# Optimization experiments

Measured on AMD Instinct MI355X. Metric: run time of the kernel, lower is better.

Reference implementation:

```python
import jax, jax.numpy as jnp
import numpy as np

HEADS = 8
HEAD_DIM = 64
SCALE = HEAD_DIM ** -0.5


def setup_inputs() -> dict:
    key = jax.random.key(0)
    ks = jax.random.split(key, 5)
    d_model, inner = 1024, HEADS * HEAD_DIM  # 512
    x = jax.random.normal(ks[0], (2, 2048, d_model), dtype=jnp.float32)
    # torch Linear weights stored pre-transposed as [in, out]
    Wq = jax.random.normal(ks[1], (d_model, inner), dtype=jnp.float32) * (d_model ** -0.5)
    Wkv = jax.random.normal(ks[2], (d_model, 2 * inner), dtype=jnp.float32) * (d_model ** -0.5)
    Wo = jax.random.normal(ks[3], (inner, d_model), dtype=jnp.float32) * (inner ** -0.5)
    bo = jnp.zeros((d_model,), dtype=jnp.float32)
    return {"x": x, "Wq": Wq, "Wkv": Wkv, "Wo": Wo, "bo": bo}


def reference(x, Wq, Wkv, Wo, bo):
    b, n, _ = x.shape
    q = x @ Wq                       # [b, n, h*d]
    kv = x @ Wkv                     # [b, n, 2*h*d] (self-attention: context = x)
    k, v = jnp.split(kv, 2, axis=-1)

    def split_heads(t):
        return t.reshape(b, n, HEADS, HEAD_DIM).transpose(0, 2, 1, 3)  # [b, h, n, d]

    q, k, v = map(split_heads, (q, k, v))
    sim = jnp.einsum('bhid,bhjd->bhij', q, k) * SCALE  # [b, h, n, n]
    attn = jax.nn.softmax(sim, axis=-1)                # dropout p=0.0 -> identity
    out = jnp.einsum('bhij,bhjd->bhid', attn, v)       # [b, h, n, d]
    out = out.transpose(0, 2, 1, 3).reshape(b, n, HEADS * HEAD_DIM)
    return out @ Wo + bo
```

## Files before the change

kernel.cpp:

```cpp
#include <hip/hip_runtime.h>

typedef _Float16 f16;
typedef __attribute__((ext_vector_type(4))) _Float16 f16x4;
typedef __attribute__((ext_vector_type(8))) _Float16 f16x8;
typedef __attribute__((ext_vector_type(4))) float f32x4;

#define CEXP 0.18033688011112042f
#define QB_LD 544
#define FIXM 12.0f

__device__ __forceinline__ void gload16(const f16* g, f16* l) {
    __builtin_amdgcn_global_load_lds((const __attribute__((address_space(1))) void*)g,
                                     (__attribute__((address_space(3))) void*)l, 16, 0, 0);
}

__global__ __launch_bounds__(256) void prep_k(const float* __restrict__ x,
                                              const float* __restrict__ Wq,
                                              const float* __restrict__ Wkv,
                                              const float* __restrict__ Wo,
                                              f16* __restrict__ xb,
                                              f16* __restrict__ wqkvT,
                                              f16* __restrict__ woT) {
    int z = blockIdx.z;
    if (z == 3) {
        size_t idx = ((size_t)(blockIdx.y * 32 + blockIdx.x) * 256 + threadIdx.x) * 16;
#pragma unroll
        for (int h = 0; h < 2; h++) {
            float4 a = *(const float4*)(x + idx + h * 8);
            float4 b = *(const float4*)(x + idx + h * 8 + 4);
            f16x8 o;
            o[0] = (f16)a.x; o[1] = (f16)a.y; o[2] = (f16)a.z; o[3] = (f16)a.w;
            o[4] = (f16)b.x; o[5] = (f16)b.y; o[6] = (f16)b.z; o[7] = (f16)b.w;
            *(f16x8*)(xb + idx + h * 8) = o;
        }
        return;
    }
    const float* in; f16* out; int N, ldo, row_off, gx, gy;
    if (z == 0)      { in = Wq;  out = wqkvT; N = 512;  ldo = 1024; row_off = 0;   gx = 16; gy = 32; }
    else if (z == 1) { in = Wkv; out = wqkvT; N = 1024; ldo = 1024; row_off = 512; gx = 32; gy = 32; }
    else             { in = Wo;  out = woT;   N = 1024; ldo = 512;  row_off = 0;   gx = 32; gy = 16; }
    if (blockIdx.x >= gx || blockIdx.y >= gy) return;

    __shared__ float tile[32][33];
    int tx = threadIdx.x & 31, ty = threadIdx.x >> 5;
    int n0 = blockIdx.x * 32, k0 = blockIdx.y * 32;
#pragma unroll
    for (int j = 0; j < 4; j++)
        tile[ty + j * 8][tx] = in[(size_t)(k0 + ty + j * 8) * N + n0 + tx];
    __syncthreads();
#pragma unroll
    for (int j = 0; j < 4; j++)
        out[(size_t)(row_off + n0 + ty + j * 8) * ldo + k0 + tx] = (f16)tile[tx][ty + j * 8];
}

template <int MODE, int BN>
__global__ __launch_bounds__(256) void gemm_k(
    const f16* __restrict__ A, const f16* __restrict__ Bt,
    f16* __restrict__ Cq, f16* __restrict__ Ckf, f16* __restrict__ Cvt,
    float* __restrict__ Cout, const float* __restrict__ bias,
    int K, int NTILES) {
    __shared__ __align__(16) f16 As[2][128 * 64];
    __shared__ __align__(16) f16 Bs[2][BN * 64];
    constexpr int MI = (BN == 128) ? 4 : 2;
    constexpr int NB = (BN == 128) ? 4 : 2;
    int bid = blockIdx.x;
    int nt = bid % NTILES, mt = bid / NTILES;
    int m0 = mt * 128, n0 = nt * BN;
    int tid = threadIdx.x;
    int lane = tid & 63, w = tid >> 6;
    int rowBase = (BN == 128) ? (w >> 1) * 64 : w * 32;
    int colBase = (BN == 128) ? (w & 1) * 64 : 0;
    int lr = lane & 15, lg = lane >> 4;
    int rowL = lane >> 3;
    int colL = (lane & 7) * 8;
    int bRow0 = (BN == 128) ? w * 32 : w * 16;
    const f16* aSrc = A + (size_t)(m0 + w * 32 + rowL) * K + colL;
    const f16* bSrc = Bt + (size_t)(n0 + bRow0 + rowL) * K + colL;
    f32x4 acc[MI][4] = {};

    auto stage = [&](int buf, int k0) {
#pragma unroll
        for (int j = 0; j < 4; j++)
            gload16(aSrc + k0 + (size_t)(j * 8) * K, &As[buf][(w * 32 + j * 8) * 64]);
#pragma unroll
        for (int j = 0; j < NB; j++)
            gload16(bSrc + k0 + (size_t)(j * 8) * K, &Bs[buf][(bRow0 + j * 8) * 64]);
    };

    stage(0, 0);
    __syncthreads();

    int KT = K >> 6;
    for (int kt = 0; kt < KT; kt++) {
        int cur = kt & 1;
        if (kt + 1 < KT) stage(cur ^ 1, (kt + 1) * 64);
#pragma unroll
        for (int ks = 0; ks < 2; ks++) {
            f16x8 af[MI], bf[4];
#pragma unroll
            for (int i = 0; i < MI; i++)
                af[i] = *(const f16x8*)(&As[cur][(rowBase + i * 16 + lr) * 64 + ks * 32 + lg * 8]);
#pragma unroll
            for (int j = 0; j < 4; j++)
                bf[j] = *(const f16x8*)(&Bs[cur][(colBase + j * 16 + lr) * 64 + ks * 32 + lg * 8]);
#pragma unroll
            for (int i = 0; i < MI; i++)
#pragma unroll
                for (int j = 0; j < 4; j++)
                    acc[i][j] = __builtin_amdgcn_mfma_f32_16x16x32_f16(af[i], bf[j], acc[i][j], 0, 0, 0);
        }
        __syncthreads();
    }

#pragma unroll
    for (int i = 0; i < MI; i++) {
#pragma unroll
        for (int j = 0; j < 4; j++) {
            int row = m0 + rowBase + i * 16 + lg * 4;
            int col = n0 + colBase + j * 16 + lr;
            if (MODE == 1) {
                float bv = bias[col];
#pragma unroll
                for (int r = 0; r < 4; r++)
                    Cout[(size_t)(row + r) * 1024 + col] = acc[i][j][r] + bv;
            } else {
                if (col < 512) {
#pragma unroll
                    for (int r = 0; r < 4; r++)
                        Cq[(size_t)(row + r) * QB_LD + col] = (f16)(acc[i][j][r] * CEXP);
                } else if (col < 1024) {
                    int c2 = col - 512;
                    int hh = c2 >> 6, d = c2 & 63;
                    int pair = (row >> 11) * 8 + hh;
                    int n = row & 2047;
                    int t = n >> 6, kvl = n & 63;
                    int kg = kvl >> 4, lrA = kvl & 15;
                    int cc = d >> 5, lgA = (d >> 3) & 3, j8 = d & 7;
                    size_t base = ((((size_t)(pair * 32 + t) * 4 + kg) * 2 + cc) * 64
                                   + lgA * 16 + lrA) * 8 + j8;
#pragma unroll
                    for (int r = 0; r < 4; r++)
                        Ckf[base + r * 8] = (f16)acc[i][j][r];
                } else {
                    int c = col - 1024;
                    int hh = c >> 6, d = c & 63;
                    int bb = row >> 11, n = row & 2047;
                    int pr = bb * 8 + hh;
                    int tt = n >> 6, kvl = n & 63;
                    int kg = kvl >> 4, lga = (kvl >> 2) & 3;
                    int dgp = d >> 5, dh = (d >> 4) & 1, lra = d & 15;
                    f16x4 ov;
#pragma unroll
                    for (int r = 0; r < 4; r++) ov[r] = (f16)acc[i][j][r];
                    size_t idx = ((((size_t)(pr * 32 + tt) * 4 + kg) * 2 + dgp) * 64
                                  + lga * 16 + lra) * 8 + dh * 4;
                    *(f16x4*)(Cvt + idx) = ov;
                }
            }
        }
    }
}

__global__ __launch_bounds__(256)
__attribute__((amdgpu_waves_per_eu(4, 4)))
void attn_k(const f16* __restrict__ qb2,
            const f16* __restrict__ kfb,
            const f16* __restrict__ vt2,
            f16* __restrict__ ao) {
    __shared__ float mO[2][64][16];
    __shared__ float mL[2][64];

    int bid = blockIdx.x;
    int xcd = bid & 7;
    int pair = xcd * 2 + ((bid >> 3) & 1);
    int qblk = bid >> 4;
    int b = pair >> 3, h = pair & 7;
    int tid = threadIdx.x;
    int lane = tid & 63, w = tid >> 6;
    int half = w >> 1, wl = w & 1;
    int lr = lane & 15, lg = lane >> 4;
    int q0 = qblk * 32 + wl * 16;

    const f16* qrow = qb2 + ((size_t)b * 2048 + q0 + lr) * QB_LD + h * 64;
    f16x8 qf0 = *(const f16x8*)(qrow + lg * 8);
    f16x8 qf1 = *(const f16x8*)(qrow + 32 + lg * 8);

    const f16* kbase = kfb + ((size_t)pair * 32) * 4096 + lane * 8;
    const f16* vbase = vt2 + ((size_t)pair * 32) * 4096 + lane * 8;
    int tg0 = half * 16;

    f16x8 kk[8], vv[8];
    {
        const f16* kp = kbase + (size_t)tg0 * 4096;
        const f16* vp = vbase + (size_t)tg0 * 4096;
#pragma unroll
        for (int u = 0; u < 8; u++) kk[u] = *(const f16x8*)(kp + u * 512);
#pragma unroll
        for (int u = 0; u < 8; u++) vv[u] = *(const f16x8*)(vp + u * 512);
    }

    f32x4 acc[4] = {};
    float lp = 0.f;

#pragma unroll 1
    for (int t = 0; t < 16; t++) {
        int tn = tg0 + ((t < 15) ? t + 1 : t);

        f32x4 s[4];
        __builtin_amdgcn_s_setprio(1);
#pragma unroll
        for (int kg = 0; kg < 4; kg++) {
            f32x4 z = {};
            z = __builtin_amdgcn_mfma_f32_16x16x32_f16(kk[kg * 2], qf0, z, 0, 0, 0);
            s[kg] = __builtin_amdgcn_mfma_f32_16x16x32_f16(kk[kg * 2 + 1], qf1, z, 0, 0, 0);
        }
        __builtin_amdgcn_s_setprio(0);

        {
            const f16* kp = kbase + (size_t)tn * 4096;
#pragma unroll
            for (int u = 0; u < 8; u++) kk[u] = *(const f16x8*)(kp + u * 512);
        }

        __builtin_amdgcn_s_setprio(1);
#pragma unroll
        for (int kg = 0; kg < 4; kg++) {
            float p0 = __builtin_amdgcn_exp2f(s[kg][0] - FIXM);
            float p1 = __builtin_amdgcn_exp2f(s[kg][1] - FIXM);
            float p2 = __builtin_amdgcn_exp2f(s[kg][2] - FIXM);
            float p3 = __builtin_amdgcn_exp2f(s[kg][3] - FIXM);
            lp += (p0 + p1) + (p2 + p3);
            f16x4 pf;
            pf[0] = (f16)p0; pf[1] = (f16)p1; pf[2] = (f16)p2; pf[3] = (f16)p3;

            f16x8 vx0 = vv[kg * 2], vx1 = vv[kg * 2 + 1];
            f16x4 v0lo = __builtin_shufflevector(vx0, vx0, 0, 1, 2, 3);
            f16x4 v0hi = __builtin_shufflevector(vx0, vx0, 4, 5, 6, 7);
            f16x4 v1lo = __builtin_shufflevector(vx1, vx1, 0, 1, 2, 3);
            f16x4 v1hi = __builtin_shufflevector(vx1, vx1, 4, 5, 6, 7);
            acc[0] = __builtin_amdgcn_mfma_f32_16x16x16f16(v0lo, pf, acc[0], 0, 0, 0);
            acc[1] = __builtin_amdgcn_mfma_f32_16x16x16f16(v0hi, pf, acc[1], 0, 0, 0);
            acc[2] = __builtin_amdgcn_mfma_f32_16x16x16f16(v1lo, pf, acc[2], 0, 0, 0);
            acc[3] = __builtin_amdgcn_mfma_f32_16x16x16f16(v1hi, pf, acc[3], 0, 0, 0);
        }
        __builtin_amdgcn_s_setprio(0);

        {
            const f16* vp = vbase + (size_t)tn * 4096;
#pragma unroll
            for (int u = 0; u < 8; u++) vv[u] = *(const f16x8*)(vp + u * 512);
        }
    }

    lp += __shfl_xor(lp, 16, 64);
    lp += __shfl_xor(lp, 32, 64);
    if (half == 1) {
#pragma unroll
        for (int dg = 0; dg < 4; dg++)
            *(f32x4*)&mO[wl][lane][dg * 4] = acc[dg];
        mL[wl][lane] = lp;
    }
    __syncthreads();
    if (half == 0) {
        float inv = 1.f / (lp + mL[wl][lane]);
#pragma unroll
        for (int dg = 0; dg < 4; dg++) {
            f32x4 oP = *(const f32x4*)&mO[wl][lane][dg * 4];
            f16x4 ov;
#pragma unroll
            for (int r = 0; r < 4; r++)
                ov[r] = (f16)((acc[dg][r] + oP[r]) * inv);
            *(f16x4*)(ao + (size_t)(b * 2048 + q0 + lr) * 512 + h * 64 + dg * 16 + lg * 4) = ov;
        }
    }
}

extern "C" void kernel_launch(void* const* d_in, const int* in_sizes, int n_in,
                              void* d_out, int out_size, void* d_ws, size_t ws_size,
                              hipStream_t stream) {
    const float* x   = (const float*)d_in[0];
    const float* Wq  = (const float*)d_in[1];
    const float* Wkv = (const float*)d_in[2];
    const float* Wo  = (const float*)d_in[3];
    const float* bo  = (const float*)d_in[4];
    float* out = (float*)d_out;

    f16* xb    = (f16*)d_ws;
    f16* wqkvT = xb + 4096 * 1024;
    f16* woT   = wqkvT + 1536 * 1024;
    f16* qb2   = woT + 1024 * 512;
    f16* kfb   = qb2 + 4096 * QB_LD;
    f16* vtb2  = kfb + 16 * 32 * 4096;
    f16* ao    = vtb2 + 16 * 32 * 4096;

    prep_k<<<dim3(32, 32, 4), 256, 0, stream>>>(x, Wq, Wkv, Wo, xb, wqkvT, woT);
    gemm_k<0, 64><<<32 * 24, 256, 0, stream>>>(xb, wqkvT, qb2, kfb, vtb2, nullptr, nullptr, 1024, 24);
    attn_k<<<1024, 256, 0, stream>>>(qb2, kfb, vtb2, ao);
    gemm_k<1, 128><<<32 * 8, 256, 0, stream>>>(ao, woT, nullptr, nullptr, nullptr, out, bo, 512, 8);
}
```

Measured before the change: 88.71 us.

## Split KV across four waves, each covering both query sub-tiles, and reduce via LDS

The attention kernel now has every wave process both 16-row query sub-tiles over its own quarter of the KV tiles (8 tiles instead of 16). Each K/V register fragment loaded from global memory is therefore reused for two query tiles, halving K/V traffic per wave. Partial outputs and row sums from all four waves are combined through a larger LDS buffer, and each wave writes one 16-column slice of the output. This doubles the accumulator and score registers, so the occupancy hint moves from waves_per_eu(4,4) to launch_bounds(256,3), which risks lower occupancy and costs a heavier final reduction.

```diff
diff --git a/kernel.cpp b/kernel.cpp
--- a/kernel.cpp
+++ b/kernel.cpp
@@ -161,14 +161,13 @@
     }
 }
 
-__global__ __launch_bounds__(256)
-__attribute__((amdgpu_waves_per_eu(4, 4)))
+__global__ __launch_bounds__(256, 3)
 void attn_k(const f16* __restrict__ qb2,
             const f16* __restrict__ kfb,
             const f16* __restrict__ vt2,
             f16* __restrict__ ao) {
-    __shared__ float mO[2][64][16];
-    __shared__ float mL[2][64];
+    __shared__ float accS[4][2][4][64][4];
+    __shared__ float lpS[4][2][64];
 
     int bid = blockIdx.x;
     int xcd = bid & 7;
@@ -177,17 +176,19 @@
     int b = pair >> 3, h = pair & 7;
     int tid = threadIdx.x;
     int lane = tid & 63, w = tid >> 6;
-    int half = w >> 1, wl = w & 1;
     int lr = lane & 15, lg = lane >> 4;
-    int q0 = qblk * 32 + wl * 16;
-
-    const f16* qrow = qb2 + ((size_t)b * 2048 + q0 + lr) * QB_LD + h * 64;
-    f16x8 qf0 = *(const f16x8*)(qrow + lg * 8);
-    f16x8 qf1 = *(const f16x8*)(qrow + 32 + lg * 8);
+    int q0 = qblk * 32;
+
+    const f16* qrowA = qb2 + ((size_t)b * 2048 + q0 + lr) * QB_LD + h * 64;
+    const f16* qrowB = qrowA + (size_t)16 * QB_LD;
+    f16x8 qfA0 = *(const f16x8*)(qrowA + lg * 8);
+    f16x8 qfA1 = *(const f16x8*)(qrowA + 32 + lg * 8);
+    f16x8 qfB0 = *(const f16x8*)(qrowB + lg * 8);
+    f16x8 qfB1 = *(const f16x8*)(qrowB + 32 + lg * 8);
 
     const f16* kbase = kfb + ((size_t)pair * 32) * 4096 + lane * 8;
     const f16* vbase = vt2 + ((size_t)pair * 32) * 4096 + lane * 8;
-    int tg0 = half * 16;
+    int tg0 = w * 8;
 
     f16x8 kk[8], vv[8];
     {
@@ -199,20 +200,26 @@
         for (int u = 0; u < 8; u++) vv[u] = *(const f16x8*)(vp + u * 512);
     }
 
-    f32x4 acc[4] = {};
-    float lp = 0.f;
+    f32x4 accA[4] = {}, accB[4] = {};
+    float lpA = 0.f, lpB = 0.f;
 
 #pragma unroll 1
-    for (int t = 0; t < 16; t++) {
-        int tn = tg0 + ((t < 15) ? t + 1 : t);
-
-        f32x4 s[4];
+    for (int t = 0; t < 8; t++) {
+        int tn = tg0 + ((t < 7) ? t + 1 : t);
+
+        f32x4 sA[4], sB[4];
         __builtin_amdgcn_s_setprio(1);
 #pragma unroll
         for (int kg = 0; kg < 4; kg++) {
             f32x4 z = {};
-            z = __builtin_amdgcn_mfma_f32_16x16x32_f16(kk[kg * 2], qf0, z, 0, 0, 0);
-            s[kg] = __builtin_amdgcn_mfma_f32_16x16x32_f16(kk[kg * 2 + 1], qf1, z, 0, 0, 0);
+            z = __builtin_amdgcn_mfma_f32_16x16x32_f16(kk[kg * 2], qfA0, z, 0, 0, 0);
+            sA[kg] = __builtin_amdgcn_mfma_f32_16x16x32_f16(kk[kg * 2 + 1], qfA1, z, 0, 0, 0);
+        }
+#pragma unroll
+        for (int kg = 0; kg < 4; kg++) {
+            f32x4 z = {};
+            z = __builtin_amdgcn_mfma_f32_16x16x32_f16(kk[kg * 2], qfB0, z, 0, 0, 0);
+            sB[kg] = __builtin_amdgcn_mfma_f32_16x16x32_f16(kk[kg * 2 + 1], qfB1, z, 0, 0, 0);
         }
         __builtin_amdgcn_s_setprio(0);
 
@@ -225,11 +232,11 @@
         __builtin_amdgcn_s_setprio(1);
 #pragma unroll
         for (int kg = 0; kg < 4; kg++) {
-            float p0 = __builtin_amdgcn_exp2f(s[kg][0] - FIXM);
-            float p1 = __builtin_amdgcn_exp2f(s[kg][1] - FIXM);
-            float p2 = __builtin_amdgcn_exp2f(s[kg][2] - FIXM);
-            float p3 = __builtin_amdgcn_exp2f(s[kg][3] - FIXM);
-            lp += (p0 + p1) + (p2 + p3);
+            float p0 = __builtin_amdgcn_exp2f(sA[kg][0] - FIXM);
+            float p1 = __builtin_amdgcn_exp2f(sA[kg][1] - FIXM);
+            float p2 = __builtin_amdgcn_exp2f(sA[kg][2] - FIXM);
+            float p3 = __builtin_amdgcn_exp2f(sA[kg][3] - FIXM);
+            lpA += (p0 + p1) + (p2 + p3);
             f16x4 pf;
             pf[0] = (f16)p0; pf[1] = (f16)p1; pf[2] = (f16)p2; pf[3] = (f16)p3;
 
@@ -238,10 +245,30 @@
             f16x4 v0hi = __builtin_shufflevector(vx0, vx0, 4, 5, 6, 7);
             f16x4 v1lo = __builtin_shufflevector(vx1, vx1, 0, 1, 2, 3);
             f16x4 v1hi = __builtin_shufflevector(vx1, vx1, 4, 5, 6, 7);
-            acc[0] = __builtin_amdgcn_mfma_f32_16x16x16f16(v0lo, pf, acc[0], 0, 0, 0);
-            acc[1] = __builtin_amdgcn_mfma_f32_16x16x16f16(v0hi, pf, acc[1], 0, 0, 0);
-            acc[2] = __builtin_amdgcn_mfma_f32_16x16x16f16(v1lo, pf, acc[2], 0, 0, 0);
-            acc[3] = __builtin_amdgcn_mfma_f32_16x16x16f16(v1hi, pf, acc[3], 0, 0, 0);
+            accA[0] = __builtin_amdgcn_mfma_f32_16x16x16f16(v0lo, pf, accA[0], 0, 0, 0);
+            accA[1] = __builtin_amdgcn_mfma_f32_16x16x16f16(v0hi, pf, accA[1], 0, 0, 0);
+            accA[2] = __builtin_amdgcn_mfma_f32_16x16x16f16(v1lo, pf, accA[2], 0, 0, 0);
+            accA[3] = __builtin_amdgcn_mfma_f32_16x16x16f16(v1hi, pf, accA[3], 0, 0, 0);
+        }
+#pragma unroll
+        for (int kg = 0; kg < 4; kg++) {
+            float p0 = __builtin_amdgcn_exp2f(sB[kg][0] - FIXM);
+            float p1 = __builtin_amdgcn_exp2f(sB[kg][1] - FIXM);
+            float p2 = __builtin_amdgcn_exp2f(sB[kg][2] - FIXM);
+            float p3 = __builtin_amdgcn_exp2f(sB[kg][3] - FIXM);
+            lpB += (p0 + p1) + (p2 + p3);
+            f16x4 pf;
+            pf[0] = (f16)p0; pf[1] = (f16)p1; pf[2] = (f16)p2; pf[3] = (f16)p3;
+
+            f16x8 vx0 = vv[kg * 2], vx1 = vv[kg * 2 + 1];
+            f16x4 v0lo = __builtin_shufflevector(vx0, vx0, 0, 1, 2, 3);
+            f16x4 v0hi = __builtin_shufflevector(vx0, vx0, 4, 5, 6, 7);
+            f16x4 v1lo = __builtin_shufflevector(vx1, vx1, 0, 1, 2, 3);
+            f16x4 v1hi = __builtin_shufflevector(vx1, vx1, 4, 5, 6, 7);
+            accB[0] = __builtin_amdgcn_mfma_f32_16x16x16f16(v0lo, pf, accB[0], 0, 0, 0);
+            accB[1] = __builtin_amdgcn_mfma_f32_16x16x16f16(v0hi, pf, accB[1], 0, 0, 0);
+            accB[2] = __builtin_amdgcn_mfma_f32_16x16x16f16(v1lo, pf, accB[2], 0, 0, 0);
+            accB[3] = __builtin_amdgcn_mfma_f32_16x16x16f16(v1hi, pf, accB[3], 0, 0, 0);
         }
         __builtin_amdgcn_s_setprio(0);
 
@@ -252,26 +279,34 @@
         }
     }
 
-    lp += __shfl_xor(lp, 16, 64);
-    lp += __shfl_xor(lp, 32, 64);
-    if (half == 1) {
-#pragma unroll
-        for (int dg = 0; dg < 4; dg++)
-            *(f32x4*)&mO[wl][lane][dg * 4] = acc[dg];
-        mL[wl][lane] = lp;
-    }
+    lpA += __shfl_xor(lpA, 16, 64);
+    lpA += __shfl_xor(lpA, 32, 64);
+    lpB += __shfl_xor(lpB, 16, 64);
+    lpB += __shfl_xor(lpB, 32, 64);
+
+#pragma unroll
+    for (int dg = 0; dg < 4; dg++) {
+        *(f32x4*)&accS[w][0][dg][lane][0] = accA[dg];
+        *(f32x4*)&accS[w][1][dg][lane][0] = accB[dg];
+    }
+    lpS[w][0][lane] = lpA;
+    lpS[w][1][lane] = lpB;
     __syncthreads();
-    if (half == 0) {
-        float inv = 1.f / (lp + mL[wl][lane]);
-#pragma unroll
-        for (int dg = 0; dg < 4; dg++) {
-            f32x4 oP = *(const f32x4*)&mO[wl][lane][dg * 4];
-            f16x4 ov;
-#pragma unroll
-            for (int r = 0; r < 4; r++)
-                ov[r] = (f16)((acc[dg][r] + oP[r]) * inv);
-            *(f16x4*)(ao + (size_t)(b * 2048 + q0 + lr) * 512 + h * 64 + dg * 16 + lg * 4) = ov;
-        }
+
+#pragma unroll
+    for (int sub = 0; sub < 2; sub++) {
+        f32x4 o = {};
+        float L = 0.f;
+#pragma unroll
+        for (int w2 = 0; w2 < 4; w2++) {
+            o += *(const f32x4*)&accS[w2][sub][w][lane][0];
+            L += lpS[w2][sub][lane];
+        }
+        float inv = 1.f / L;
+        f16x4 ov;
+#pragma unroll
+        for (int r = 0; r < 4; r++) ov[r] = (f16)(o[r] * inv);
+        *(f16x4*)(ao + (size_t)(b * 2048 + q0 + sub * 16 + lr) * 512 + h * 64 + w * 16 + lg * 4) = ov;
     }
 }
 
```

Result: faster. 84.37 us (-4.9%).
